# Kernel optimization log

Measured on AMD Instinct MI355X. Metric: run time of the kernel, lower is better.

## Reference

```python
import jax, jax.numpy as jnp
import numpy as np

RADIUS = 5
ALPHA = 200.0
N, H, W = 8, 352, 352


def _maxpool5(x):
    # F.max_pool2d(kernel=5, stride=1, padding=2); torch pads with -inf for max pool
    return jax.lax.reduce_window(
        x, -jnp.inf, jax.lax.max,
        window_dimensions=(1, 1, 5, 5), window_strides=(1, 1, 1, 1),
        padding=[(0, 0), (0, 0), (2, 2), (2, 2)])


def setup_inputs() -> dict:
    key = jax.random.key(0)
    k1, k2 = jax.random.split(key)
    pred = jax.random.uniform(k1, (N, 1, H, W), dtype=jnp.float32)
    feat = jax.random.uniform(k2, (N, 3, H, W), dtype=jnp.float32)
    return {"pred": pred, "feat": feat}


def reference(pred, feat):
    # interpolate(pred, scale_factor=1.0) and interpolate(feat, size=pred HxW)
    # are identities here (same spatial size, bilinear align_corners).
    sal_map = pred
    image_ = feat

    # contour mask: dilation - erosion of thresholded saliency
    lbl = (sal_map > 0.5).astype(sal_map.dtype)
    ero = 1.0 - _maxpool5(1.0 - lbl)
    dil = _maxpool5(lbl)
    mask = dil - ero  # (N,1,H,W)

    features = jnp.concatenate([image_, sal_map], axis=1)  # (N,4,H,W)
    n, c, h, w = features.shape
    r = RADIUS
    # zero padding matches F.unfold's implicit zero padding
    fpad = jnp.pad(features, ((0, 0), (0, 0), (r, r), (r, r)))
    center_rgb = features[:, :3]   # (N,3,H,W)
    center_sal = features[:, 3:]   # (N,1,H,W)

    # On-the-fly sliding-window reduction instead of materializing the
    # (N,4,11,11,H,W) unfold tensor. 121 static shifts (fixed small set).
    loss_map = jnp.zeros((n, 1, h, w), dtype=features.dtype)
    for dy in range(2 * r + 1):
        for dx in range(2 * r + 1):
            win = fpad[:, :, dy:dy + h, dx:dx + w]  # (N,4,H,W)
            d_rgb = win[:, :3] - center_rgb
            d_sal = jnp.abs(win[:, 3:] - center_sal)
            wgt = jnp.exp(-ALPHA * jnp.sum(d_rgb * d_rgb, axis=1, keepdims=True))
            loss_map = loss_map + wgt * d_sal

    loss = jnp.sum(loss_map * mask) / (jnp.sum(mask) + 1e-6)
    return loss
```

## Files before the change

### kernel.cpp

```cpp
#include <hip/hip_runtime.h>

#define NB 8
#define HH 352
#define WW 352
#define TX 32
#define TY 32
#define TLH 37
#define TLW 42
#define LSTRIDE 43
#define SLH 41
#define SLW 46
#define SSTRIDE 47
#define MH 37
#define MW 42
#define MSTRIDE 44
#define TILES_X 11
#define TILES_Y 11
#define NBLK (TILES_X * TILES_Y * NB)

#define RGB_SCALE 16.98644781888824f

typedef float f32x2 __attribute__((ext_vector_type(2)));

__device__ __forceinline__ float elem(float4 q, int c) {
    return c == 0 ? q.x : c == 1 ? q.y : c == 2 ? q.z : q.w;
}

__device__ __forceinline__ void tap_pair(const float4& w, float mq,
                                         f32x2 ncx, f32x2 ncy, f32x2 ncz, f32x2 ncw,
                                         f32x2& accP, f32x2& accQ) {
    f32x2 d0 = ncx + w.x;
    f32x2 d1 = ncy + w.y;
    f32x2 d2 = ncz + w.z;
    f32x2 s  = d0 * d0;
    s += d1 * d1;
    s += d2 * d2;
    f32x2 ds = ncw + w.w;
    f32x2 v;
    v.x = __builtin_amdgcn_exp2f(-s.x) * fabsf(ds.x);
    v.y = __builtin_amdgcn_exp2f(-s.y) * fabsf(ds.y);
    accP += v;
    f32x2 mqv; mqv.x = mq; mqv.y = mq;
    accQ += v * mqv;
}

__device__ __forceinline__ void tap_scalar(const float4& w, float mq,
                                           float ncx, float ncy, float ncz, float ncw,
                                           float& aP, float& aQ) {
    float d0 = w.x + ncx, d1 = w.y + ncy, d2 = w.z + ncz;
    float s = fmaf(d0, d0, fmaf(d1, d1, d2 * d2));
    float v = __builtin_amdgcn_exp2f(-s) * fabsf(w.w + ncw);
    aP += v;
    aQ = fmaf(v, mq, aQ);
}

template <bool INTERIOR>
__device__ __forceinline__ void mask_plane_fn(const float* __restrict__ salp,
                                              float* __restrict__ maskp,
                                              int y0, int x0, int t) {
    for (int i = t; i < MH * MW; i += 256) {
        int mr = i / MW, mc = i - mr * MW;
        int gy = y0 + mr, gx = x0 - 5 + mc;
        float m = 0.f;
        if (INTERIOR || (gy < HH && (unsigned)gx < (unsigned)WW)) {
            float mx = 0.f, mn = 1.f;
            #pragma unroll
            for (int r = 0; r < 5; ++r) {
                bool rowv = INTERIOR || ((unsigned)(gy - 2 + r) < (unsigned)HH);
                const float* sr = &salp[(mr + r) * SSTRIDE + mc];
                #pragma unroll
                for (int c = 0; c < 5; ++c) {
                    float sv = sr[c];
                    mx = fmaxf(mx, sv);
                    bool ok = INTERIOR || (rowv && ((unsigned)(gx - 2 + c) < (unsigned)WW));
                    mn = fminf(mn, ok ? sv : 1.f);
                }
            }
            m = (mx > 0.5f ? 1.f : 0.f) - (mn > 0.5f ? 1.f : 0.f);
        }
        maskp[mr * MSTRIDE + mc] = m;
    }
}

__global__ __launch_bounds__(256, 2)
void btm_loss_kernel(const float* __restrict__ pred,
                     const float* __restrict__ feat,
                     float2* __restrict__ partials) {
    __shared__ __align__(16) float4 tile[TLH * LSTRIDE];
    __shared__ __align__(16) float  salp[SLH * SSTRIDE];
    __shared__ __align__(16) float  maskp[MH * MSTRIDE];
    __shared__ float2 wred[4];

    const int bid = blockIdx.x;
    const int tx_blk = bid % TILES_X;
    const int ty_blk = (bid / TILES_X) % TILES_Y;
    const int n = bid / (TILES_X * TILES_Y);
    const int x0 = tx_blk * TX;
    const int y0 = ty_blk * TY;

    const size_t plane = (size_t)HH * WW;
    const float* fr = feat + ((size_t)n * 3 + 0) * plane;
    const float* fg = feat + ((size_t)n * 3 + 1) * plane;
    const float* fb = feat + ((size_t)n * 3 + 2) * plane;
    const float* ps = pred + (size_t)n * plane;

    for (int i = threadIdx.x; i < SLH * SLW; i += 256) {
        int lr = i / SLW;
        int lc = i - lr * SLW;
        int gy = y0 + lr - 2;
        int gx = x0 + lc - 7;
        float s = 0.f;
        if ((unsigned)gy < (unsigned)HH && (unsigned)gx < (unsigned)WW)
            s = ps[gy * WW + gx];
        salp[lr * SSTRIDE + lc] = s;
    }
    for (int i = threadIdx.x; i < TLH * TLW; i += 256) {
        int lr = i / TLW;
        int lc = i - lr * TLW;
        int gy = y0 + lr;
        int gx = x0 + lc - 5;
        float4 v = make_float4(0.f, 0.f, 0.f, 0.f);
        if ((unsigned)gy < (unsigned)HH && (unsigned)gx < (unsigned)WW) {
            int gi = gy * WW + gx;
            v.x = fr[gi] * RGB_SCALE;
            v.y = fg[gi] * RGB_SCALE;
            v.z = fb[gi] * RGB_SCALE;
            v.w = ps[gi];
        }
        tile[lr * LSTRIDE + lc] = v;
    }
    __syncthreads();

    const bool interior = (tx_blk >= 1) && (tx_blk <= TILES_X - 2) &&
                          (ty_blk >= 1) && (ty_blk <= TILES_Y - 2);
    if (interior) mask_plane_fn<true >(salp, maskp, y0, x0, threadIdx.x);
    else          mask_plane_fn<false>(salp, maskp, y0, x0, threadIdx.x);
    __syncthreads();

    const int t   = threadIdx.x;
    const int txq = t & 7;
    const int ty  = t >> 3;
    const int px0 = txq * 4;

    const float4* trow = tile + ty * LSTRIDE + px0;
    const float*  mrow = maskp + ty * MSTRIDE + px0;

    float4 c0 = trow[5], c1 = trow[6], c2 = trow[7], c3 = trow[8];
    f32x2 n01x = {-c0.x, -c1.x}, n01y = {-c0.y, -c1.y}, n01z = {-c0.z, -c1.z}, n01w = {-c0.w, -c1.w};
    f32x2 n23x = {-c2.x, -c3.x}, n23y = {-c2.y, -c3.y}, n23z = {-c2.z, -c3.z}, n23w = {-c2.w, -c3.w};

    f32x2 aP01 = {0.f, 0.f}, aP23 = {0.f, 0.f};
    f32x2 aQ01 = {0.f, 0.f}, aQ23 = {0.f, 0.f};
    float sP0 = 0.f, sP1 = 0.f, sP2 = 0.f, sP3 = 0.f, sQ = 0.f;

    float4 mf0[3];
    #pragma unroll
    for (int q = 0; q < 3; ++q) mf0[q] = *(const float4*)&mrow[4 + 4 * q];
    {
        float4 w0[8];
        #pragma unroll
        for (int j = 0; j < 8; ++j) w0[j] = trow[6 + j];

        tap_scalar(w0[0], elem(mf0[0], 2), n01x.x, n01y.x, n01z.x, n01w.x, sP0, sQ);
        #pragma unroll
        for (int j = 1; j <= 4; ++j)
            tap_pair(w0[j], elem(mf0[(j + 2) >> 2], (j + 2) & 3), n01x, n01y, n01z, n01w, aP01, aQ01);
        tap_scalar(w0[5], elem(mf0[1], 3), n01x.y, n01y.y, n01z.y, n01w.y, sP1, sQ);
        tap_scalar(w0[2], elem(mf0[1], 0), n23x.x, n23y.x, n23z.x, n23w.x, sP2, sQ);
        #pragma unroll
        for (int j = 3; j <= 6; ++j)
            tap_pair(w0[j], elem(mf0[(j + 2) >> 2], (j + 2) & 3), n23x, n23y, n23z, n23w, aP23, aQ23);
        tap_scalar(w0[7], elem(mf0[2], 1), n23x.y, n23y.y, n23z.y, n23w.y, sP3, sQ);
    }

    #pragma unroll 1
    for (int dy = 1; dy <= 5; ++dy) {
        float4 w[14];
        #pragma unroll
        for (int j = 0; j < 14; ++j) w[j] = trow[dy * LSTRIDE + j];
        float4 mf[4];
        const float* mro = mrow + dy * MSTRIDE;
        #pragma unroll
        for (int q = 0; q < 4; ++q) mf[q] = *(const float4*)&mro[4 * q];

        tap_scalar(w[0], elem(mf[0], 0), n01x.x, n01y.x, n01z.x, n01w.x, sP0, sQ);
        #pragma unroll
        for (int j = 1; j <= 10; ++j)
            tap_pair(w[j], elem(mf[j >> 2], j & 3), n01x, n01y, n01z, n01w, aP01, aQ01);
        tap_scalar(w[11], elem(mf[2], 3), n01x.y, n01y.y, n01z.y, n01w.y, sP1, sQ);
        tap_scalar(w[2],  elem(mf[0], 2), n23x.x, n23y.x, n23z.x, n23w.x, sP2, sQ);
        #pragma unroll
        for (int j = 3; j <= 12; ++j)
            tap_pair(w[j], elem(mf[j >> 2], j & 3), n23x, n23y, n23z, n23w, aP23, aQ23);
        tap_scalar(w[13], elem(mf[3], 1), n23x.y, n23y.y, n23z.y, n23w.y, sP3, sQ);
    }

    float m0 = mf0[0].y, m1 = mf0[0].z, m2 = mf0[0].w, m3 = mf0[1].x;
    float e0 = aP01.x + sP0, e1 = aP01.y + sP1;
    float e2 = aP23.x + sP2, e3 = aP23.y + sP3;

    const bool padblk = (ty_blk == 0) || (tx_blk == 0) || (tx_blk == TILES_X - 1);
    if (padblk) {
        const int gy = y0 + ty;
        const int nneg = (5 - gy) > 0 ? (5 - gy) : 0;
        #pragma unroll
        for (int i = 0; i < 4; ++i) {
            const int gx = x0 + px0 + i;
            const int cl = (5 - gx) > 0 ? (5 - gx) : 0;
            const int cr = (gx - 346) > 0 ? (gx - 346) : 0;
            const int np = nneg * 11 + (5 - nneg) * (cl + cr) + cl;
            if (np > 0) {
                float4 ci = (i == 0) ? c0 : (i == 1) ? c1 : (i == 2) ? c2 : c3;
                float s2 = fmaf(ci.x, ci.x, fmaf(ci.y, ci.y, ci.z * ci.z));
                float vp = __builtin_amdgcn_exp2f(-s2) * ci.w * (float)np;
                if (i == 0) e0 += vp; else if (i == 1) e1 += vp;
                else if (i == 2) e2 += vp; else e3 += vp;
            }
        }
    }

    float num = fmaf(m0, e0, fmaf(m1, e1, fmaf(m2, e2, m3 * e3)))
              + ((aQ01.x + aQ01.y) + (aQ23.x + aQ23.y)) + sQ;
    float den = (m0 + m1) + (m2 + m3);

    #pragma unroll
    for (int off = 32; off > 0; off >>= 1) {
        num += __shfl_down(num, off, 64);
        den += __shfl_down(den, off, 64);
    }
    const int wid  = t >> 6;
    const int lane = t & 63;
    if (lane == 0) wred[wid] = make_float2(num, den);
    __syncthreads();
    if (t == 0) {
        float2 a = wred[0];
        #pragma unroll
        for (int w2 = 1; w2 < 4; ++w2) { a.x += wred[w2].x; a.y += wred[w2].y; }
        partials[bid] = a;
    }
}

__global__ __launch_bounds__(256)
void btm_finalize_kernel(const float2* __restrict__ partials,
                         float* __restrict__ out) {
    __shared__ float2 wred[4];
    float num = 0.f, den = 0.f;
    for (int i = threadIdx.x; i < NBLK; i += 256) {
        float2 p = partials[i];
        num += p.x;
        den += p.y;
    }
    #pragma unroll
    for (int off = 32; off > 0; off >>= 1) {
        num += __shfl_down(num, off, 64);
        den += __shfl_down(den, off, 64);
    }
    int wid  = threadIdx.x >> 6;
    int lane = threadIdx.x & 63;
    if (lane == 0) wred[wid] = make_float2(num, den);
    __syncthreads();
    if (threadIdx.x == 0) {
        float2 a = wred[0];
        #pragma unroll
        for (int w = 1; w < 4; ++w) { a.x += wred[w].x; a.y += wred[w].y; }
        out[0] = a.x / (a.y + 1e-6f);
    }
}

extern "C" void kernel_launch(void* const* d_in, const int* in_sizes, int n_in,
                              void* d_out, int out_size, void* d_ws, size_t ws_size,
                              hipStream_t stream) {
    const float* pred = (const float*)d_in[0];
    const float* feat = (const float*)d_in[1];
    float* out = (float*)d_out;
    float2* partials = (float2*)d_ws;

    btm_loss_kernel<<<dim3(NBLK), dim3(256), 0, stream>>>(pred, feat, partials);
    btm_finalize_kernel<<<dim3(1), dim3(256), 0, stream>>>(partials, out);
}
```

Baseline: 96.92 us.

## Compute contour mask with wavefront ballot bitmasks and fuse finalize via last-block atomic

Replaces the per-pixel 5x5 min/max mask computation over a shared saliency plane with wavefront ballots that build per-row bitmasks of thresholded values. Horizontal dilation is done with shifts and vertical dilation with ORs of five rows. The contour mask is then the AND of the dilated foreground and dilated background masks. The separate finalize kernel is removed: a global counter and atomicAdd let the last block reduce the partials. This adds a memset launch, threadfences and an atomic, and it relies on the workspace being large enough for the counter at its fixed offset.

```diff
diff --git a/kernel.cpp b/kernel.cpp
--- a/kernel.cpp
+++ b/kernel.cpp
@@ -8,9 +8,6 @@
 #define TLH 37
 #define TLW 42
 #define LSTRIDE 43
-#define SLH 41
-#define SLW 46
-#define SSTRIDE 47
 #define MH 37
 #define MW 42
 #define MSTRIDE 44
@@ -54,42 +51,19 @@
     aQ = fmaf(v, mq, aQ);
 }
 
-template <bool INTERIOR>
-__device__ __forceinline__ void mask_plane_fn(const float* __restrict__ salp,
-                                              float* __restrict__ maskp,
-                                              int y0, int x0, int t) {
-    for (int i = t; i < MH * MW; i += 256) {
-        int mr = i / MW, mc = i - mr * MW;
-        int gy = y0 + mr, gx = x0 - 5 + mc;
-        float m = 0.f;
-        if (INTERIOR || (gy < HH && (unsigned)gx < (unsigned)WW)) {
-            float mx = 0.f, mn = 1.f;
-            #pragma unroll
-            for (int r = 0; r < 5; ++r) {
-                bool rowv = INTERIOR || ((unsigned)(gy - 2 + r) < (unsigned)HH);
-                const float* sr = &salp[(mr + r) * SSTRIDE + mc];
-                #pragma unroll
-                for (int c = 0; c < 5; ++c) {
-                    float sv = sr[c];
-                    mx = fmaxf(mx, sv);
-                    bool ok = INTERIOR || (rowv && ((unsigned)(gx - 2 + c) < (unsigned)WW));
-                    mn = fminf(mn, ok ? sv : 1.f);
-                }
-            }
-            m = (mx > 0.5f ? 1.f : 0.f) - (mn > 0.5f ? 1.f : 0.f);
-        }
-        maskp[mr * MSTRIDE + mc] = m;
-    }
-}
-
 __global__ __launch_bounds__(256, 2)
 void btm_loss_kernel(const float* __restrict__ pred,
                      const float* __restrict__ feat,
-                     float2* __restrict__ partials) {
+                     float2* __restrict__ partials,
+                     unsigned* __restrict__ counter,
+                     float* __restrict__ out) {
     __shared__ __align__(16) float4 tile[TLH * LSTRIDE];
-    __shared__ __align__(16) float  salp[SLH * SSTRIDE];
     __shared__ __align__(16) float  maskp[MH * MSTRIDE];
+    __shared__ unsigned long long hbuf[41];
+    __shared__ unsigned long long nhbuf[41];
+    __shared__ unsigned long long Mbuf[37];
     __shared__ float2 wred[4];
+    __shared__ int islast;
 
     const int bid = blockIdx.x;
     const int tx_blk = bid % TILES_X;
@@ -104,17 +78,25 @@
     const float* fb = feat + ((size_t)n * 3 + 2) * plane;
     const float* ps = pred + (size_t)n * plane;
 
-    for (int i = threadIdx.x; i < SLH * SLW; i += 256) {
-        int lr = i / SLW;
-        int lc = i - lr * SLW;
-        int gy = y0 + lr - 2;
-        int gx = x0 + lc - 7;
-        float s = 0.f;
-        if ((unsigned)gy < (unsigned)HH && (unsigned)gx < (unsigned)WW)
-            s = ps[gy * WW + gx];
-        salp[lr * SSTRIDE + lc] = s;
-    }
-    for (int i = threadIdx.x; i < TLH * TLW; i += 256) {
+    const int t = threadIdx.x;
+
+    {
+        const int wv = t >> 6, ln = t & 63;
+        for (int r = wv; r < 41; r += 4) {
+            int gy = y0 + r - 2;
+            int gx = x0 - 7 + ln;
+            bool inimg = ((unsigned)gy < (unsigned)HH) &&
+                         ((unsigned)gx < (unsigned)WW) && (ln < 46);
+            float sv = inimg ? ps[gy * WW + gx] : 0.f;
+            unsigned long long lb = __ballot(inimg && (sv > 0.5f));
+            unsigned long long nb = __ballot(inimg && (sv <= 0.5f));
+            unsigned long long a2 = lb | (lb >> 1); a2 |= (a2 >> 2); a2 |= (lb >> 4);
+            unsigned long long b2 = nb | (nb >> 1); b2 |= (b2 >> 2); b2 |= (nb >> 4);
+            if (ln == 0) { hbuf[r] = a2; nhbuf[r] = b2; }
+        }
+    }
+
+    for (int i = t; i < TLH * TLW; i += 256) {
         int lr = i / TLW;
         int lc = i - lr * TLW;
         int gy = y0 + lr;
@@ -131,13 +113,23 @@
     }
     __syncthreads();
 
-    const bool interior = (tx_blk >= 1) && (tx_blk <= TILES_X - 2) &&
-                          (ty_blk >= 1) && (ty_blk <= TILES_Y - 2);
-    if (interior) mask_plane_fn<true >(salp, maskp, y0, x0, threadIdx.x);
-    else          mask_plane_fn<false>(salp, maskp, y0, x0, threadIdx.x);
-    __syncthreads();
-
-    const int t   = threadIdx.x;
+    if (t < 37) {
+        int lo = 5 - x0; if (lo < 0) lo = 0;
+        int hi = WW + 5 - x0; if (hi > 42) hi = 42;
+        unsigned long long cm = ((1ull << hi) - 1) & ~((1ull << lo) - 1);
+        unsigned long long D = hbuf[t], E = nhbuf[t];
+        #pragma unroll
+        for (int k = 1; k < 5; ++k) { D |= hbuf[t + k]; E |= nhbuf[t + k]; }
+        Mbuf[t] = (y0 + t < HH) ? (D & E & cm) : 0ull;
+    }
+    __syncthreads();
+
+    for (int i = t; i < MH * MW; i += 256) {
+        int mr = i / MW, mc = i - mr * MW;
+        maskp[mr * MSTRIDE + mc] = (float)((Mbuf[mr] >> mc) & 1ull);
+    }
+    __syncthreads();
+
     const int txq = t & 7;
     const int ty  = t >> 3;
     const int px0 = txq * 4;
@@ -237,33 +229,33 @@
         #pragma unroll
         for (int w2 = 1; w2 < 4; ++w2) { a.x += wred[w2].x; a.y += wred[w2].y; }
         partials[bid] = a;
-    }
-}
-
-__global__ __launch_bounds__(256)
-void btm_finalize_kernel(const float2* __restrict__ partials,
-                         float* __restrict__ out) {
-    __shared__ float2 wred[4];
-    float num = 0.f, den = 0.f;
-    for (int i = threadIdx.x; i < NBLK; i += 256) {
-        float2 p = partials[i];
-        num += p.x;
-        den += p.y;
-    }
-    #pragma unroll
-    for (int off = 32; off > 0; off >>= 1) {
-        num += __shfl_down(num, off, 64);
-        den += __shfl_down(den, off, 64);
-    }
-    int wid  = threadIdx.x >> 6;
-    int lane = threadIdx.x & 63;
-    if (lane == 0) wred[wid] = make_float2(num, den);
-    __syncthreads();
-    if (threadIdx.x == 0) {
-        float2 a = wred[0];
-        #pragma unroll
-        for (int w = 1; w < 4; ++w) { a.x += wred[w].x; a.y += wred[w].y; }
-        out[0] = a.x / (a.y + 1e-6f);
+        __threadfence();
+        unsigned old = atomicAdd(counter, 1u);
+        islast = (old == (unsigned)(NBLK - 1)) ? 1 : 0;
+    }
+    __syncthreads();
+
+    if (islast) {
+        __threadfence();
+        float fn = 0.f, fd = 0.f;
+        for (int i = t; i < NBLK; i += 256) {
+            float2 p = partials[i];
+            fn += p.x;
+            fd += p.y;
+        }
+        #pragma unroll
+        for (int off = 32; off > 0; off >>= 1) {
+            fn += __shfl_down(fn, off, 64);
+            fd += __shfl_down(fd, off, 64);
+        }
+        if (lane == 0) wred[wid] = make_float2(fn, fd);
+        __syncthreads();
+        if (t == 0) {
+            float2 a = wred[0];
+            #pragma unroll
+            for (int w2 = 1; w2 < 4; ++w2) { a.x += wred[w2].x; a.y += wred[w2].y; }
+            out[0] = a.x / (a.y + 1e-6f);
+        }
     }
 }
 
@@ -274,7 +266,9 @@
     const float* feat = (const float*)d_in[1];
     float* out = (float*)d_out;
     float2* partials = (float2*)d_ws;
-
-    btm_loss_kernel<<<dim3(NBLK), dim3(256), 0, stream>>>(pred, feat, partials);
-    btm_finalize_kernel<<<dim3(1), dim3(256), 0, stream>>>(partials, out);
-}
+    unsigned* counter = (unsigned*)((char*)d_ws + 8192);
+
+    hipMemsetAsync(counter, 0, sizeof(unsigned), stream);
+    btm_loss_kernel<<<dim3(NBLK), dim3(256), 0, stream>>>(pred, feat, partials,
+                                                          counter, out);
+}
```

Result: slower. 109.1 us (+12.6%).
